# Performance work log

Measured on AMD Instinct MI355X. Metric: run time of the kernel, lower is better.

Reference implementation:

```python
import jax, jax.numpy as jnp
import numpy as np

B, T, F, U = 256, 512, 128, 512

def setup_inputs() -> dict:
    key = jax.random.key(0)
    ks = jax.random.split(key, 9)
    g = lambda k, shape, s: jax.random.normal(k, shape, dtype=jnp.float32) * s
    s_in = float(np.sqrt(2.0 / (F + U)))   # glorot-ish scale for input kernels
    s_u = float(np.sqrt(1.0 / U))          # recurrent kernel scale
    inputs = g(ks[0], (B, T, F + 1), 1.0)
    # make trailing interval column non-negative (time gaps)
    inputs = inputs.at[:, :, -1].set(jnp.abs(inputs[:, :, -1]))
    return {
        "inputs": inputs,
        "h0": jnp.zeros((B, U), jnp.float32),
        "w_z": g(ks[1], (F, U), s_in), "u_z": g(ks[2], (U, U), s_u), "b_z": jnp.zeros((1,), jnp.float32),
        "w_r": g(ks[3], (F, U), s_in), "u_r": g(ks[4], (U, U), s_u), "b_r": jnp.zeros((1,), jnp.float32),
        "w_h": g(ks[5], (F, U), s_in), "u_h": g(ks[6], (U, U), s_u), "b_h": jnp.zeros((1,), jnp.float32),
        "w_int": jnp.abs(g(ks[7], (1, U), 0.1)),  # NonNeg constraint
        "b_int": jnp.zeros((1,), jnp.float32),
    }

def reference(inputs, h0, w_z, u_z, b_z, w_r, u_r, b_r, w_h, u_h, b_h, w_int, b_int):
    # GRU-D style cell: last input column is the time interval driving an exp decay.
    def step(h, xt):
        x = xt[:, :-1]                 # [B, F]
        interval = xt[:, -1:]          # [B, 1]
        decay = jnp.exp(-jax.nn.relu(interval * w_int + b_int))      # [B, U]
        z = jax.nn.sigmoid(x @ w_z + h @ u_z + b_z)
        r = jax.nn.sigmoid(x @ w_r + h @ u_r + b_r)
        h_hat = jnp.tanh(x @ w_h + (h * r) @ u_h + b_h)
        h_new = decay * (z * h + (1.0 - z) * h_hat)
        return h_new, h_new
    xs = jnp.swapaxes(inputs, 0, 1)    # [T, B, F+1]
    _, ys = jax.lax.scan(step, h0, xs)
    return jnp.swapaxes(ys, 0, 1)      # [B, T, U]
```

## Files before the change

### kernel.cpp

```cpp
#include <hip/hip_runtime.h>

#define Bn 256
#define Tn 512
#define Fn 128
#define Un 512
#define XFn 129
#define BM 16
#define GC 16
#define NG 16
#define XS 136
#define HS 520
#define KT 20

typedef __attribute__((ext_vector_type(8))) short short8;
typedef __attribute__((ext_vector_type(4))) float floatx4;
typedef unsigned long long ull;

__device__ __forceinline__ unsigned short f2bf(float f) {
  unsigned u = __float_as_uint(f);
  u += 0x7fffu + ((u >> 16) & 1u);
  return (unsigned short)(u >> 16);
}
__device__ __forceinline__ float bf2f(unsigned v) {
  return __uint_as_float((v & 0xffffu) << 16);
}

__device__ __forceinline__ ull ldc8(const void* p) {
  return __hip_atomic_load((const ull*)p, __ATOMIC_RELAXED, __HIP_MEMORY_SCOPE_AGENT);
}
__device__ __forceinline__ void stc8(void* p, ull v) {
  __hip_atomic_store((ull*)p, v, __ATOMIC_RELAXED, __HIP_MEMORY_SCOPE_AGENT);
}
__device__ __forceinline__ ull pack4(float a, float b, float c, float d) {
  return (ull)f2bf(a) | ((ull)f2bf(b) << 16) | ((ull)f2bf(c) << 32) | ((ull)f2bf(d) << 48);
}

__device__ __forceinline__ void group_barrier(unsigned* cnt, unsigned target) {
  __syncthreads();
  if (threadIdx.x == 0) {
    __hip_atomic_fetch_add(cnt, 1u, __ATOMIC_RELAXED, __HIP_MEMORY_SCOPE_AGENT);
    while (__hip_atomic_load(cnt, __ATOMIC_RELAXED, __HIP_MEMORY_SCOPE_AGENT) < target)
      __builtin_amdgcn_s_sleep(1);
  }
  __syncthreads();
}

__global__ void zero_counters(unsigned* c) { c[threadIdx.x] = 0u; }


__global__ __launch_bounds__(256, 1)
void gru_kernel(const float* __restrict__ inp, const float* __restrict__ h0,
                const float* __restrict__ wz, const float* __restrict__ uz, const float* __restrict__ bz_,
                const float* __restrict__ wr, const float* __restrict__ ur, const float* __restrict__ br_,
                const float* __restrict__ wh, const float* __restrict__ uh, const float* __restrict__ bh_,
                const float* __restrict__ wint_, const float* __restrict__ bint_,
                float* __restrict__ out,
                unsigned short* __restrict__ h_buf, unsigned short* __restrict__ r_buf,
                unsigned* __restrict__ counters)
{
  __shared__ short Xlds[2][16 * XS];
  __shared__ short Hlds[16 * HS];
  __shared__ float ivals[2][16];

  const int tid  = threadIdx.x;
  const int wave = tid >> 6;
  const int lane = tid & 63;
  const int ln   = lane & 15;
  const int quad = lane >> 4;
  const int g    = blockIdx.x & 15;
  const int wg   = blockIdx.x >> 4;

  unsigned* cnt = counters + g * 16;
  unsigned short* rg = r_buf + (size_t)g * (Un * BM);
  unsigned short* hg = h_buf + (size_t)g * (Un * BM);

  const float* gw1 = (wave < 2) ? wz : wr;
  const float* gu1 = (wave < 2) ? uz : ur;
  const int ncol1 = wg * 32 + (wave & 1) * 16 + ln;
  short8 bf1[KT];
  #pragma unroll
  for (int kk = 0; kk < KT; ++kk) {
    short8 v;
    #pragma unroll
    for (int j = 0; j < 8; ++j) {
      int k = kk * 32 + quad * 8 + j;
      float w = (k < Fn) ? gw1[k * Un + ncol1] : gu1[(k - Fn) * Un + ncol1];
      v[j] = (short)f2bf(w);
    }
    bf1[kk] = v;
  }
  const int ncol2 = wg * 32 + wave * 16 + ln;
  short8 bf2[KT];
  if (wave < 2) {
    #pragma unroll
    for (int kk = 0; kk < KT; ++kk) {
      short8 v;
      #pragma unroll
      for (int j = 0; j < 8; ++j) {
        int k = kk * 32 + quad * 8 + j;
        float w = (k < Fn) ? wh[k * Un + ncol2] : uh[(k - Fn) * Un + ncol2];
        v[j] = (short)f2bf(w);
      }
      bf2[kk] = v;
    }
  }

  const float bz = bz_[0], br = br_[0], bh = bh_[0], bint = bint_[0];
  const float wint = (wave < 2) ? wint_[ncol2] : 0.f;

  float hold[4] = {0.f, 0.f, 0.f, 0.f};
  if (wave < 2) {
    #pragma unroll
    for (int i = 0; i < 4; ++i)
      hold[i] = h0[(size_t)(g * BM + quad * 4 + i) * Un + ncol2];
  }

  {
    int row = tid >> 4, ch = tid & 15;
    const float* xr = inp + ((size_t)(g * BM + row) * Tn + 0) * XFn + ch * 8;
    short8 v;
    #pragma unroll
    for (int j = 0; j < 8; ++j) v[j] = (short)f2bf(xr[j]);
    *(short8*)&Xlds[0][row * XS + ch * 8] = v;
    if (tid < 16)
      ivals[0][tid] = inp[((size_t)(g * BM + tid) * Tn + 0) * XFn + Fn];
    const float* hp = h0 + (size_t)(g * BM + row) * Un + ch * 32;
    #pragma unroll
    for (int s = 0; s < 4; ++s) {
      short8 hv;
      #pragma unroll
      for (int j = 0; j < 8; ++j) hv[j] = (short)f2bf(hp[s * 8 + j]);
      *(short8*)&Hlds[row * HS + ch * 32 + s * 8] = hv;
    }
  }

  for (int t = 0; t < Tn; ++t) {
    const int buf = t & 1;

    if (t > 0) {
      const int c0 = tid * 2;
      ull ha[4], hb[4];
      #pragma unroll
      for (int q = 0; q < 4; ++q) ha[q] = ldc8(hg + (size_t)c0 * BM + q * 4);
      #pragma unroll
      for (int q = 0; q < 4; ++q) hb[q] = ldc8(hg + (size_t)(c0 + 1) * BM + q * 4);
      #pragma unroll
      for (int r = 0; r < 16; ++r) {
        unsigned lo = (unsigned)((ha[r >> 2] >> ((r & 3) * 16)) & 0xffffu);
        unsigned hi = (unsigned)((hb[r >> 2] >> ((r & 3) * 16)) & 0xffffu);
        *(unsigned*)&Hlds[r * HS + c0] = lo | (hi << 16);
      }
    }
    __syncthreads();

    floatx4 a0 = {0.f,0.f,0.f,0.f}, a1 = {0.f,0.f,0.f,0.f};
    {
      const short* xb = &Xlds[buf][ln * XS + quad * 8];
      const short* hb = &Hlds[ln * HS + quad * 8];
      #pragma unroll
      for (int kk = 0; kk < KT; ++kk) {
        const short* ap = (kk < 4) ? (xb + kk * 32) : (hb + (kk - 4) * 32);
        short8 a = *(const short8*)ap;
        if (kk & 1) a1 = __builtin_amdgcn_mfma_f32_16x16x32_bf16(a, bf1[kk], a1, 0, 0, 0);
        else        a0 = __builtin_amdgcn_mfma_f32_16x16x32_bf16(a, bf1[kk], a0, 0, 0, 0);
      }
    }
    float zf[4];
    {
      floatx4 acc = a0 + a1;
      if (wave < 2) {
        #pragma unroll
        for (int i = 0; i < 4; ++i) zf[i] = 1.f / (1.f + __expf(-(acc[i] + bz)));
      } else {
        float rv[4];
        #pragma unroll
        for (int i = 0; i < 4; ++i) rv[i] = 1.f / (1.f + __expf(-(acc[i] + br)));
        stc8(rg + (size_t)ncol1 * BM + quad * 4, pack4(rv[0], rv[1], rv[2], rv[3]));
      }
    }

    group_barrier(cnt, (unsigned)(GC * (2 * t + 1)));

    {
      const int c0 = tid * 2;
      ull ra[4], rb[4];
      #pragma unroll
      for (int q = 0; q < 4; ++q) ra[q] = ldc8(rg + (size_t)c0 * BM + q * 4);
      #pragma unroll
      for (int q = 0; q < 4; ++q) rb[q] = ldc8(rg + (size_t)(c0 + 1) * BM + q * 4);
      #pragma unroll
      for (int r = 0; r < 16; ++r) {
        unsigned hv = *(unsigned*)&Hlds[r * HS + c0];
        float p0 = bf2f(hv) * bf2f((unsigned)(ra[r >> 2] >> ((r & 3) * 16)));
        float p1 = bf2f(hv >> 16) * bf2f((unsigned)(rb[r >> 2] >> ((r & 3) * 16)));
        *(unsigned*)&Hlds[r * HS + c0] = (unsigned)f2bf(p0) | ((unsigned)f2bf(p1) << 16);
      }
    }
    __syncthreads();

    if (wave < 2) {
      floatx4 b0 = {0.f,0.f,0.f,0.f}, b1 = {0.f,0.f,0.f,0.f};
      const short* xb = &Xlds[buf][ln * XS + quad * 8];
      const short* hb = &Hlds[ln * HS + quad * 8];
      #pragma unroll
      for (int kk = 0; kk < KT; ++kk) {
        const short* ap = (kk < 4) ? (xb + kk * 32) : (hb + (kk - 4) * 32);
        short8 a = *(const short8*)ap;
        if (kk & 1) b1 = __builtin_amdgcn_mfma_f32_16x16x32_bf16(a, bf2[kk], b1, 0, 0, 0);
        else        b0 = __builtin_amdgcn_mfma_f32_16x16x32_bf16(a, bf2[kk], b0, 0, 0, 0);
      }
      floatx4 acc2 = b0 + b1;
      float hn[4];
      #pragma unroll
      for (int i = 0; i < 4; ++i) {
        int m = quad * 4 + i;
        float hh  = 1.f - 2.f / (__expf(2.f * (acc2[i] + bh)) + 1.f);
        float dec = __expf(-fmaxf(ivals[buf][m] * wint + bint, 0.f));
        float v   = dec * (zf[i] * hold[i] + (1.f - zf[i]) * hh);
        hold[i] = v; hn[i] = v;
        out[((size_t)(g * BM + m) * Tn + t) * Un + ncol2] = v;
      }
      stc8(hg + (size_t)ncol2 * BM + quad * 4, pack4(hn[0], hn[1], hn[2], hn[3]));
    } else if (t + 1 < Tn) {
      int id = tid - 128;
      int row = id >> 3, ch = id & 7;
      const float* xr = inp + ((size_t)(g * BM + row) * Tn + (t + 1)) * XFn + ch * 16;
      short8 v0, v1;
      #pragma unroll
      for (int j = 0; j < 8; ++j) { v0[j] = (short)f2bf(xr[j]); v1[j] = (short)f2bf(xr[8 + j]); }
      *(short8*)&Xlds[buf ^ 1][row * XS + ch * 16]     = v0;
      *(short8*)&Xlds[buf ^ 1][row * XS + ch * 16 + 8] = v1;
      if (id < 16)
        ivals[buf ^ 1][id] = inp[((size_t)(g * BM + id) * Tn + (t + 1)) * XFn + Fn];
    }

    group_barrier(cnt, (unsigned)(GC * (2 * t + 2)));
  }
}

extern "C" void kernel_launch(void* const* d_in, const int* in_sizes, int n_in,
                              void* d_out, int out_size, void* d_ws, size_t ws_size,
                              hipStream_t stream) {
  const float* inp  = (const float*)d_in[0];
  const float* h0   = (const float*)d_in[1];
  const float* wz   = (const float*)d_in[2];
  const float* uz   = (const float*)d_in[3];
  const float* bz   = (const float*)d_in[4];
  const float* wr   = (const float*)d_in[5];
  const float* ur   = (const float*)d_in[6];
  const float* br   = (const float*)d_in[7];
  const float* wh   = (const float*)d_in[8];
  const float* uh   = (const float*)d_in[9];
  const float* bh   = (const float*)d_in[10];
  const float* wint = (const float*)d_in[11];
  const float* bint = (const float*)d_in[12];
  float* out = (float*)d_out;

  unsigned* counters    = (unsigned*)d_ws;
  unsigned short* r_buf = (unsigned short*)((char*)d_ws + 1024);
  unsigned short* h_buf = (unsigned short*)((char*)d_ws + 1024 + (size_t)Bn * Un * 2);

  hipLaunchKernelGGL(zero_counters, dim3(1), dim3(256), 0, stream, counters);

  void* args[] = {(void*)&inp, (void*)&h0, (void*)&wz, (void*)&uz, (void*)&bz,
                  (void*)&wr, (void*)&ur, (void*)&br, (void*)&wh, (void*)&uh,
                  (void*)&bh, (void*)&wint, (void*)&bint, (void*)&out,
                  (void*)&h_buf, (void*)&r_buf, (void*)&counters};
  hipError_t e = hipLaunchCooperativeKernel((void*)gru_kernel, dim3(NG * GC), dim3(256),
                                            args, 0, stream);
  if (e != hipSuccess) {
    hipLaunchKernelGGL(gru_kernel, dim3(NG * GC), dim3(256), 0, stream,
                       inp, h0, wz, uz, bz, wr, ur, br, wh, uh, bh, wint, bint,
                       out, h_buf, r_buf, counters);
  }
}
```

Baseline: 3.151 ms.

## Replace group counter barriers with per-wave flag polling and precomputed h*r exchange

The shared atomic counter barriers are replaced with per-wave flags. Each producer wave sets its own flag after storing, and consumers poll all 32 flags of their group with a wave-wide vote. The r-gate waves now compute h*r locally and publish the product, so consumers gather it directly into a second LDS buffer instead of re-multiplying. The output store moves after the flag signal, and the MFMA chains use four accumulators instead of two. This removes serialized atomic increments and one barrier round-trip per step. The cost is more polling traffic and relaxed-ordering correctness that depends on the explicit waitcnt before each flag store.

```diff
diff --git a/kernel.cpp b/kernel.cpp
--- a/kernel.cpp
+++ b/kernel.cpp
@@ -24,6 +24,9 @@
 __device__ __forceinline__ float bf2f(unsigned v) {
   return __uint_as_float((v & 0xffffu) << 16);
 }
+__device__ __forceinline__ ull pack4(float a, float b, float c, float d) {
+  return (ull)f2bf(a) | ((ull)f2bf(b) << 16) | ((ull)f2bf(c) << 32) | ((ull)f2bf(d) << 48);
+}
 
 __device__ __forceinline__ ull ldc8(const void* p) {
   return __hip_atomic_load((const ull*)p, __ATOMIC_RELAXED, __HIP_MEMORY_SCOPE_AGENT);
@@ -31,22 +34,34 @@
 __device__ __forceinline__ void stc8(void* p, ull v) {
   __hip_atomic_store((ull*)p, v, __ATOMIC_RELAXED, __HIP_MEMORY_SCOPE_AGENT);
 }
-__device__ __forceinline__ ull pack4(float a, float b, float c, float d) {
-  return (ull)f2bf(a) | ((ull)f2bf(b) << 16) | ((ull)f2bf(c) << 32) | ((ull)f2bf(d) << 48);
-}
-
-__device__ __forceinline__ void group_barrier(unsigned* cnt, unsigned target) {
-  __syncthreads();
-  if (threadIdx.x == 0) {
-    __hip_atomic_fetch_add(cnt, 1u, __ATOMIC_RELAXED, __HIP_MEMORY_SCOPE_AGENT);
-    while (__hip_atomic_load(cnt, __ATOMIC_RELAXED, __HIP_MEMORY_SCOPE_AGENT) < target)
-      __builtin_amdgcn_s_sleep(1);
-  }
-  __syncthreads();
-}
-
-__global__ void zero_counters(unsigned* c) { c[threadIdx.x] = 0u; }
-
+
+__device__ __forceinline__ void poll32(const unsigned* flags, unsigned tgt) {
+  const unsigned* p = flags + (threadIdx.x & 31);
+  for (;;) {
+    unsigned f = __hip_atomic_load(p, __ATOMIC_RELAXED, __HIP_MEMORY_SCOPE_AGENT);
+    if (__all((int)(f >= tgt))) return;
+    __builtin_amdgcn_s_sleep(1);
+  }
+}
+
+__device__ __forceinline__ void gather_T(short* dst, const unsigned short* src) {
+  const int c0 = (int)threadIdx.x * 2;
+  const ull* q = (const ull*)(src + (size_t)c0 * BM);
+  ull v[8];
+  #pragma unroll
+  for (int i = 0; i < 8; ++i) v[i] = ldc8(q + i);
+  #pragma unroll
+  for (int r = 0; r < 16; ++r) {
+    unsigned lo = (unsigned)((v[r >> 2]       >> ((r & 3) * 16)) & 0xffffu);
+    unsigned hi = (unsigned)((v[4 + (r >> 2)] >> ((r & 3) * 16)) & 0xffffu);
+    *(unsigned*)&dst[r * HS + c0] = lo | (hi << 16);
+  }
+}
+
+__global__ void init_ws(unsigned* w) {
+  int i = blockIdx.x * 256 + threadIdx.x;
+  if (i < 1024) w[i] = 0u;
+}
 
 __global__ __launch_bounds__(256, 1)
 void gru_kernel(const float* __restrict__ inp, const float* __restrict__ h0,
@@ -55,11 +70,12 @@
                 const float* __restrict__ wh, const float* __restrict__ uh, const float* __restrict__ bh_,
                 const float* __restrict__ wint_, const float* __restrict__ bint_,
                 float* __restrict__ out,
-                unsigned short* __restrict__ h_buf, unsigned short* __restrict__ r_buf,
-                unsigned* __restrict__ counters)
+                unsigned short* __restrict__ h_buf, unsigned short* __restrict__ hr_buf,
+                unsigned* __restrict__ flags)
 {
   __shared__ short Xlds[2][16 * XS];
-  __shared__ short Hlds[16 * HS];
+  __shared__ short Ah[16 * HS];
+  __shared__ short Bh[16 * HS];
   __shared__ float ivals[2][16];
 
   const int tid  = threadIdx.x;
@@ -70,9 +86,9 @@
   const int g    = blockIdx.x & 15;
   const int wg   = blockIdx.x >> 4;
 
-  unsigned* cnt = counters + g * 16;
-  unsigned short* rg = r_buf + (size_t)g * (Un * BM);
-  unsigned short* hg = h_buf + (size_t)g * (Un * BM);
+  unsigned* gflags = flags + g * 64;
+  unsigned short* hrg = hr_buf + (size_t)g * (Un * BM);
+  unsigned short* hg  = h_buf  + (size_t)g * (Un * BM);
 
   const float* gw1 = (wave < 2) ? wz : wr;
   const float* gu1 = (wave < 2) ? uz : ur;
@@ -130,7 +146,7 @@
       short8 hv;
       #pragma unroll
       for (int j = 0; j < 8; ++j) hv[j] = (short)f2bf(hp[s * 8 + j]);
-      *(short8*)&Hlds[row * HS + ch * 32 + s * 8] = hv;
+      *(short8*)&Ah[row * HS + ch * 32 + s * 8] = hv;
     }
   }
 
@@ -138,78 +154,72 @@
     const int buf = t & 1;
 
     if (t > 0) {
-      const int c0 = tid * 2;
-      ull ha[4], hb[4];
-      #pragma unroll
-      for (int q = 0; q < 4; ++q) ha[q] = ldc8(hg + (size_t)c0 * BM + q * 4);
-      #pragma unroll
-      for (int q = 0; q < 4; ++q) hb[q] = ldc8(hg + (size_t)(c0 + 1) * BM + q * 4);
-      #pragma unroll
-      for (int r = 0; r < 16; ++r) {
-        unsigned lo = (unsigned)((ha[r >> 2] >> ((r & 3) * 16)) & 0xffffu);
-        unsigned hi = (unsigned)((hb[r >> 2] >> ((r & 3) * 16)) & 0xffffu);
-        *(unsigned*)&Hlds[r * HS + c0] = lo | (hi << 16);
-      }
+      poll32(gflags, (unsigned)t);
+      gather_T(Ah, hg);
     }
     __syncthreads();
 
     floatx4 a0 = {0.f,0.f,0.f,0.f}, a1 = {0.f,0.f,0.f,0.f};
+    floatx4 a2 = {0.f,0.f,0.f,0.f}, a3 = {0.f,0.f,0.f,0.f};
     {
       const short* xb = &Xlds[buf][ln * XS + quad * 8];
-      const short* hb = &Hlds[ln * HS + quad * 8];
+      const short* hb = &Ah[ln * HS + quad * 8];
       #pragma unroll
       for (int kk = 0; kk < KT; ++kk) {
         const short* ap = (kk < 4) ? (xb + kk * 32) : (hb + (kk - 4) * 32);
         short8 a = *(const short8*)ap;
-        if (kk & 1) a1 = __builtin_amdgcn_mfma_f32_16x16x32_bf16(a, bf1[kk], a1, 0, 0, 0);
-        else        a0 = __builtin_amdgcn_mfma_f32_16x16x32_bf16(a, bf1[kk], a0, 0, 0, 0);
+        switch (kk & 3) {
+          case 0: a0 = __builtin_amdgcn_mfma_f32_16x16x32_bf16(a, bf1[kk], a0, 0, 0, 0); break;
+          case 1: a1 = __builtin_amdgcn_mfma_f32_16x16x32_bf16(a, bf1[kk], a1, 0, 0, 0); break;
+          case 2: a2 = __builtin_amdgcn_mfma_f32_16x16x32_bf16(a, bf1[kk], a2, 0, 0, 0); break;
+          default:a3 = __builtin_amdgcn_mfma_f32_16x16x32_bf16(a, bf1[kk], a3, 0, 0, 0); break;
+        }
       }
     }
     float zf[4];
     {
-      floatx4 acc = a0 + a1;
+      floatx4 acc = (a0 + a1) + (a2 + a3);
       if (wave < 2) {
         #pragma unroll
         for (int i = 0; i < 4; ++i) zf[i] = 1.f / (1.f + __expf(-(acc[i] + bz)));
       } else {
-        float rv[4];
+        float hrv[4];
         #pragma unroll
-        for (int i = 0; i < 4; ++i) rv[i] = 1.f / (1.f + __expf(-(acc[i] + br)));
-        stc8(rg + (size_t)ncol1 * BM + quad * 4, pack4(rv[0], rv[1], rv[2], rv[3]));
-      }
-    }
-
-    group_barrier(cnt, (unsigned)(GC * (2 * t + 1)));
-
-    {
-      const int c0 = tid * 2;
-      ull ra[4], rb[4];
-      #pragma unroll
-      for (int q = 0; q < 4; ++q) ra[q] = ldc8(rg + (size_t)c0 * BM + q * 4);
-      #pragma unroll
-      for (int q = 0; q < 4; ++q) rb[q] = ldc8(rg + (size_t)(c0 + 1) * BM + q * 4);
-      #pragma unroll
-      for (int r = 0; r < 16; ++r) {
-        unsigned hv = *(unsigned*)&Hlds[r * HS + c0];
-        float p0 = bf2f(hv) * bf2f((unsigned)(ra[r >> 2] >> ((r & 3) * 16)));
-        float p1 = bf2f(hv >> 16) * bf2f((unsigned)(rb[r >> 2] >> ((r & 3) * 16)));
-        *(unsigned*)&Hlds[r * HS + c0] = (unsigned)f2bf(p0) | ((unsigned)f2bf(p1) << 16);
-      }
-    }
+        for (int i = 0; i < 4; ++i) {
+          float rv = 1.f / (1.f + __expf(-(acc[i] + br)));
+          float rb = bf2f((unsigned)f2bf(rv));
+          unsigned hv = (unsigned short)Ah[(quad * 4 + i) * HS + ncol1];
+          hrv[i] = bf2f(hv) * rb;
+        }
+        stc8(hrg + (size_t)ncol1 * BM + quad * 4,
+             pack4(hrv[0], hrv[1], hrv[2], hrv[3]));
+        asm volatile("s_waitcnt vmcnt(0)" ::: "memory");
+        if (lane == 0)
+          __hip_atomic_store(&gflags[32 + wg * 2 + (wave & 1)], (unsigned)(t + 1),
+                             __ATOMIC_RELAXED, __HIP_MEMORY_SCOPE_AGENT);
+      }
+    }
+    poll32(gflags + 32, (unsigned)(t + 1));
+    gather_T(Bh, hrg);
     __syncthreads();
 
     if (wave < 2) {
       floatx4 b0 = {0.f,0.f,0.f,0.f}, b1 = {0.f,0.f,0.f,0.f};
+      floatx4 b2 = {0.f,0.f,0.f,0.f}, b3 = {0.f,0.f,0.f,0.f};
       const short* xb = &Xlds[buf][ln * XS + quad * 8];
-      const short* hb = &Hlds[ln * HS + quad * 8];
+      const short* hb = &Bh[ln * HS + quad * 8];
       #pragma unroll
       for (int kk = 0; kk < KT; ++kk) {
         const short* ap = (kk < 4) ? (xb + kk * 32) : (hb + (kk - 4) * 32);
         short8 a = *(const short8*)ap;
-        if (kk & 1) b1 = __builtin_amdgcn_mfma_f32_16x16x32_bf16(a, bf2[kk], b1, 0, 0, 0);
-        else        b0 = __builtin_amdgcn_mfma_f32_16x16x32_bf16(a, bf2[kk], b0, 0, 0, 0);
-      }
-      floatx4 acc2 = b0 + b1;
+        switch (kk & 3) {
+          case 0: b0 = __builtin_amdgcn_mfma_f32_16x16x32_bf16(a, bf2[kk], b0, 0, 0, 0); break;
+          case 1: b1 = __builtin_amdgcn_mfma_f32_16x16x32_bf16(a, bf2[kk], b1, 0, 0, 0); break;
+          case 2: b2 = __builtin_amdgcn_mfma_f32_16x16x32_bf16(a, bf2[kk], b2, 0, 0, 0); break;
+          default:b3 = __builtin_amdgcn_mfma_f32_16x16x32_bf16(a, bf2[kk], b3, 0, 0, 0); break;
+        }
+      }
+      floatx4 acc2 = (b0 + b1) + (b2 + b3);
       float hn[4];
       #pragma unroll
       for (int i = 0; i < 4; ++i) {
@@ -218,9 +228,18 @@
         float dec = __expf(-fmaxf(ivals[buf][m] * wint + bint, 0.f));
         float v   = dec * (zf[i] * hold[i] + (1.f - zf[i]) * hh);
         hold[i] = v; hn[i] = v;
-        out[((size_t)(g * BM + m) * Tn + t) * Un + ncol2] = v;
-      }
-      stc8(hg + (size_t)ncol2 * BM + quad * 4, pack4(hn[0], hn[1], hn[2], hn[3]));
+      }
+      stc8(hg + (size_t)ncol2 * BM + quad * 4,
+           pack4(hn[0], hn[1], hn[2], hn[3]));
+      asm volatile("s_waitcnt vmcnt(0)" ::: "memory");
+      if (lane == 0)
+        __hip_atomic_store(&gflags[wg * 2 + wave], (unsigned)(t + 1),
+                           __ATOMIC_RELAXED, __HIP_MEMORY_SCOPE_AGENT);
+      #pragma unroll
+      for (int i = 0; i < 4; ++i) {
+        int m = quad * 4 + i;
+        out[((size_t)(g * BM + m) * Tn + t) * Un + ncol2] = hn[i];
+      }
     } else if (t + 1 < Tn) {
       int id = tid - 128;
       int row = id >> 3, ch = id & 7;
@@ -234,7 +253,7 @@
         ivals[buf ^ 1][id] = inp[((size_t)(g * BM + id) * Tn + (t + 1)) * XFn + Fn];
     }
 
-    group_barrier(cnt, (unsigned)(GC * (2 * t + 2)));
+    __syncthreads();
   }
 }
 
@@ -256,21 +275,21 @@
   const float* bint = (const float*)d_in[12];
   float* out = (float*)d_out;
 
-  unsigned* counters    = (unsigned*)d_ws;
-  unsigned short* r_buf = (unsigned short*)((char*)d_ws + 1024);
-  unsigned short* h_buf = (unsigned short*)((char*)d_ws + 1024 + (size_t)Bn * Un * 2);
-
-  hipLaunchKernelGGL(zero_counters, dim3(1), dim3(256), 0, stream, counters);
+  unsigned* flags       = (unsigned*)d_ws;
+  unsigned short* h_buf = (unsigned short*)((char*)d_ws + 8192);
+  unsigned short* hr_buf= (unsigned short*)((char*)d_ws + 8192 + (size_t)Bn * Un * 2);
+
+  hipLaunchKernelGGL(init_ws, dim3(4), dim3(256), 0, stream, flags);
 
   void* args[] = {(void*)&inp, (void*)&h0, (void*)&wz, (void*)&uz, (void*)&bz,
                   (void*)&wr, (void*)&ur, (void*)&br, (void*)&wh, (void*)&uh,
                   (void*)&bh, (void*)&wint, (void*)&bint, (void*)&out,
-                  (void*)&h_buf, (void*)&r_buf, (void*)&counters};
+                  (void*)&h_buf, (void*)&hr_buf, (void*)&flags};
   hipError_t e = hipLaunchCooperativeKernel((void*)gru_kernel, dim3(NG * GC), dim3(256),
                                             args, 0, stream);
   if (e != hipSuccess) {
     hipLaunchKernelGGL(gru_kernel, dim3(NG * GC), dim3(256), 0, stream,
                        inp, h0, wz, uz, bz, wr, ur, br, wh, uh, bh, wint, bint,
-                       out, h_buf, r_buf, counters);
-  }
-}
+                       out, h_buf, hr_buf, flags);
+  }
+}
```

Result: slower. 3.991 ms (+26.7%).
